# Kernel tuning notes

Hardware: AMD Instinct MI355X
Metric: run time of the kernel (lower is better)

## Reference

```python
import jax, jax.numpy as jnp
import numpy as np

B, F, T, K = 131072, 1024, 100, 32  # batch, num_features, num_trees, features per tree (sqrt(F))


def setup_inputs() -> dict:
    key = jax.random.key(0)
    kx, kw = jax.random.split(key)
    x = jax.random.normal(kx, (B, F), dtype=jnp.float32)
    # per-tree random feature selection without replacement (np.random.choice replace=False)
    rng = np.random.default_rng(0)
    idx = np.argsort(rng.random((T, F)), axis=1)[:, :K].astype(np.int32)
    feature_indices = jnp.asarray(idx)
    feature_thresholds = jnp.zeros((T, K), dtype=jnp.float32)  # lazy-init zeros in original
    feature_weights = jax.random.uniform(kw, (T, K), dtype=jnp.float32)  # torch.rand
    return {
        "x": x,
        "feature_indices": feature_indices,
        "feature_thresholds": feature_thresholds,
        "feature_weights": feature_weights,
    }


def reference(x, feature_indices, feature_thresholds, feature_weights):
    # Per tree t: ws_t = sum_k (x[:, idx[t,k]] - thr[t,k]) * w[t,k]
    # Equivalent fused form: scatter weights into a dense [T, F] matrix and do one GEMM,
    # with per-tree bias sum_k thr*w. scatter-add handles any duplicate indices identically
    # to the gather-then-sum formulation.
    T_, K_ = feature_indices.shape
    tree_ids = jnp.arange(T_, dtype=feature_indices.dtype)[:, None]  # [T,1]
    W_full = jnp.zeros((T_, x.shape[1]), dtype=x.dtype).at[tree_ids, feature_indices].add(feature_weights)
    bias = jnp.sum(feature_thresholds * feature_weights, axis=1)  # [T]
    ws = x @ W_full.T - bias[None, :]  # [B, T]
    p = jax.nn.sigmoid(ws)
    pm = jnp.mean(p, axis=1)  # mean over trees; mean(1-p) = 1 - mean(p)
    return jnp.stack([1.0 - pm, pm], axis=1)  # [B, 2]
```

## Files before the change

### kernel.cpp

```cpp
#include <hip/hip_runtime.h>
#include <math.h>

constexpr int Bn = 131072;
constexpr int Fn = 1024;
constexpr int Tn = 100;
constexpr int Kn = 32;

constexpr int TP = 112;
constexpr int NF = TP / 16;
constexpr int BK = 64;
constexpr int KS = BK / 32;
constexpr int NT = Fn / BK;
constexpr int BM = 128;
constexpr int MW = 32;
constexpr int BLOCK = 256;
constexpr int GRID = Bn / BM;

typedef __attribute__((ext_vector_type(8))) short bf16x8;
typedef __attribute__((ext_vector_type(4))) float f32x4;

using gptr_t = const __attribute__((address_space(1))) void*;
using lptr_t = __attribute__((address_space(3))) void*;

__device__ inline unsigned short f2bf(float f) {
    uint32_t u = __float_as_uint(f);
    return (unsigned short)((u + 0x7FFFu + ((u >> 16) & 1u)) >> 16);
}

__global__ __launch_bounds__(64)
void rf_prep(const int* __restrict__ fidx, const float* __restrict__ fthr,
             const float* __restrict__ fw,
             unsigned short* __restrict__ wt, float* __restrict__ bias)
{
    const int t    = blockIdx.x;
    const int lane = threadIdx.x;

    int4 z = make_int4(0, 0, 0, 0);
    int4* rowp = (int4*)(wt + (size_t)t * Fn);
    rowp[lane * 2 + 0] = z;
    rowp[lane * 2 + 1] = z;
    __syncthreads();

    float bsum = 0.f;
    if (t < Tn && lane < Kn) {
        const int   idx = fidx[t * Kn + lane];
        const float w   = fw[t * Kn + lane];
        const float th  = fthr[t * Kn + lane];
        wt[(size_t)t * Fn + idx] = f2bf(w);
        bsum = th * w;
    }
#pragma unroll
    for (int d = 1; d < 64; d <<= 1) bsum += __shfl_xor(bsum, d, 64);
    if (lane == 0) bias[t] = (t < Tn) ? bsum : 0.f;
}

__global__ __launch_bounds__(BLOCK, 2)
void rf_gemm(const float* __restrict__ x,
             const unsigned short* __restrict__ wt,
             const float* __restrict__ bias,
             float* __restrict__ out)
{
    __shared__ float lds[2][BM * BK];

    const int lane = threadIdx.x & 63;
    const int wid  = threadIdx.x >> 6;
    const int rb   = blockIdx.x * BM;

    const int s_r = lane >> 4;
    const int s_p = lane & 15;
    const int a_L = lane & 15;
    const int a_g = lane >> 4;

    f32x4 acc[2][NF];
#pragma unroll
    for (int m = 0; m < 2; ++m)
#pragma unroll
        for (int f = 0; f < NF; ++f) acc[m][f] = (f32x4){0.f, 0.f, 0.f, 0.f};

    auto stage = [&](int t, int bsel) {
#pragma unroll
        for (int i = 0; i < 8; ++i) {
            const int row = i * 4 + s_r;
            const int c   = s_p ^ (row & 15);
            const float* src = x + (size_t)(rb + wid * MW + row) * Fn + t * BK + c * 4;
            float* dst = &lds[bsel][wid * (MW * BK) + i * 256];
            __builtin_amdgcn_global_load_lds((gptr_t)src, (lptr_t)dst, 16, 0, 0);
        }
    };

    auto loadB = [&](int t, bf16x8 (&bfr)[KS][NF]) {
#pragma unroll
        for (int ks = 0; ks < KS; ++ks)
#pragma unroll
            for (int f = 0; f < NF; ++f) {
                const unsigned short* bp =
                    wt + (size_t)(f * 16 + a_L) * Fn + t * BK + ks * 32 + a_g * 8;
                bfr[ks][f] = *(const bf16x8*)bp;
            }
    };

    auto readA = [&](int bsel, bf16x8 (&af)[KS][2]) {
        const float* buf = &lds[bsel][wid * (MW * BK)];
#pragma unroll
        for (int ks = 0; ks < KS; ++ks)
#pragma unroll
            for (int m = 0; m < 2; ++m) {
                const float* rp = buf + (m * 16 + a_L) * BK;
                const int c0 = ks * 8 + a_g * 2;
                float4 lo = *(const float4*)(rp + ((c0 ^ a_L) * 4));
                float4 hi = *(const float4*)(rp + (((c0 + 1) ^ a_L) * 4));
                bf16x8 v;
                v[0] = (short)f2bf(lo.x); v[1] = (short)f2bf(lo.y);
                v[2] = (short)f2bf(lo.z); v[3] = (short)f2bf(lo.w);
                v[4] = (short)f2bf(hi.x); v[5] = (short)f2bf(hi.y);
                v[6] = (short)f2bf(hi.z); v[7] = (short)f2bf(hi.w);
                af[ks][m] = v;
            }
    };

    auto mfma_all = [&](bf16x8 (&af)[KS][2], bf16x8 (&bfr)[KS][NF]) {
#pragma unroll
        for (int ks = 0; ks < KS; ++ks)
#pragma unroll
            for (int m = 0; m < 2; ++m)
#pragma unroll
                for (int f = 0; f < NF; ++f)
                    acc[m][f] = __builtin_amdgcn_mfma_f32_16x16x32_bf16(
                        af[ks][m], bfr[ks][f], acc[m][f], 0, 0, 0);
    };

    bf16x8 bA[KS][NF], bB[KS][NF];
    bf16x8 af[KS][2];

    stage(0, 0);
    __builtin_amdgcn_sched_barrier(0);
    loadB(0, bA);
    __builtin_amdgcn_sched_barrier(0);
    stage(1, 1);

    for (int t = 0; t < NT; t += 2) {
        loadB(t + 1, bB);
        asm volatile("s_waitcnt vmcnt(36)" ::: "memory");
        readA(0, af);
        asm volatile("s_waitcnt lgkmcnt(0)" ::: "memory");
        if (t + 2 < NT) stage(t + 2, 0);
        mfma_all(af, bA);

        if (t + 2 < NT) {
            loadB(t + 2, bA);
            asm volatile("s_waitcnt vmcnt(36)" ::: "memory");
        } else {
            asm volatile("s_waitcnt vmcnt(14)" ::: "memory");
        }
        readA(1, af);
        asm volatile("s_waitcnt lgkmcnt(0)" ::: "memory");
        if (t + 3 < NT) stage(t + 3, 1);
        mfma_all(af, bB);
    }

    const int col = lane & 15;
    float psum[2][4] = {};
#pragma unroll
    for (int f = 0; f < NF; ++f) {
        const int  n     = f * 16 + col;
        const bool valid = n < Tn;
        const float bv   = bias[n];
#pragma unroll
        for (int m = 0; m < 2; ++m)
#pragma unroll
            for (int r = 0; r < 4; ++r) {
                const float ws = acc[m][f][r] - bv;
                const float p  = 1.f / (1.f + __expf(-ws));
                if (valid) psum[m][r] += p;
            }
    }
#pragma unroll
    for (int m = 0; m < 2; ++m)
#pragma unroll
        for (int r = 0; r < 4; ++r)
#pragma unroll
            for (int d = 1; d < 16; d <<= 1)
                psum[m][r] += __shfl_xor(psum[m][r], d, 64);

    const int g = lane >> 4;
#pragma unroll
    for (int m = 0; m < 2; ++m) {
        if (col < 4) {
            const int r   = col;
            const int row = rb + wid * MW + m * 16 + g * 4 + r;
            const float pm = psum[m][r] * (1.0f / Tn);
            *(float2*)(out + (size_t)row * 2) = make_float2(1.0f - pm, pm);
        }
    }
}

extern "C" void kernel_launch(void* const* d_in, const int* in_sizes, int n_in,
                              void* d_out, int out_size, void* d_ws, size_t ws_size,
                              hipStream_t stream) {
    const float* x    = (const float*)d_in[0];
    const int*   fidx = (const int*)  d_in[1];
    const float* fthr = (const float*)d_in[2];
    const float* fw   = (const float*)d_in[3];
    float*       out  = (float*)d_out;

    unsigned short* wt   = (unsigned short*)d_ws;
    float*          bias = (float*)((char*)d_ws + (size_t)TP * Fn * 2);

    rf_prep<<<TP, 64, 0, stream>>>(fidx, fthr, fw, wt, bias);
    rf_gemm<<<GRID, BLOCK, 0, stream>>>(x, wt, bias, out);
}
```

Baseline: 159.3 us.

## Stage A through registers instead of direct global-to-LDS loads, stagger tile order

Replaces the global_load_lds staging of x tiles with ordinary global loads into registers followed by explicit LDS stores, rebuilding the software pipeline around register-held prefetches with new waitcnt thresholds. Each block also starts its K loop at a different tile offset so concurrent blocks spread their reads over different columns of x and the weight matrix. B fragments are now loaded into a single buffer just before use, and A is converted per k-step. This raises register pressure and removes the explicit syncthreads-free direct LDS path. The hand-tuned vmcnt counts may not match the new load counts.

```diff
diff --git a/kernel.cpp b/kernel.cpp
--- a/kernel.cpp
+++ b/kernel.cpp
@@ -19,9 +19,6 @@
 typedef __attribute__((ext_vector_type(8))) short bf16x8;
 typedef __attribute__((ext_vector_type(4))) float f32x4;
 
-using gptr_t = const __attribute__((address_space(1))) void*;
-using lptr_t = __attribute__((address_space(3))) void*;
-
 __device__ inline unsigned short f2bf(float f) {
     uint32_t u = __float_as_uint(f);
     return (unsigned short)((u + 0x7FFFu + ((u >> 16) & 1u)) >> 16);
@@ -65,97 +62,110 @@
     const int lane = threadIdx.x & 63;
     const int wid  = threadIdx.x >> 6;
     const int rb   = blockIdx.x * BM;
-
-    const int s_r = lane >> 4;
-    const int s_p = lane & 15;
+    const int tofs = blockIdx.x & (NT - 1);
+
+    const int s_sub = lane >> 4;
+    const int s_c   = lane & 15;
     const int a_L = lane & 15;
     const int a_g = lane >> 4;
 
+    int waddr[8];
+#pragma unroll
+    for (int i = 0; i < 8; ++i) {
+        const int row  = i * 4 + s_sub;
+        const int phys = s_c ^ (row & 15);
+        waddr[i] = wid * (MW * BK * 4) + row * (BK * 4) + phys * 16;
+    }
+
     f32x4 acc[2][NF];
 #pragma unroll
     for (int m = 0; m < 2; ++m)
 #pragma unroll
         for (int f = 0; f < NF; ++f) acc[m][f] = (f32x4){0.f, 0.f, 0.f, 0.f};
 
-    auto stage = [&](int t, int bsel) {
-#pragma unroll
-        for (int i = 0; i < 8; ++i) {
-            const int row = i * 4 + s_r;
-            const int c   = s_p ^ (row & 15);
-            const float* src = x + (size_t)(rb + wid * MW + row) * Fn + t * BK + c * 4;
-            float* dst = &lds[bsel][wid * (MW * BK) + i * 256];
-            __builtin_amdgcn_global_load_lds((gptr_t)src, (lptr_t)dst, 16, 0, 0);
-        }
+    auto tileof = [&](int t) { return (t + tofs) & (NT - 1); };
+
+    auto issueA = [&](int t, float4 (&R)[8]) {
+        const float* base = x + (size_t)(rb + wid * MW) * Fn + tileof(t) * BK;
+#pragma unroll
+        for (int i = 0; i < 8; ++i)
+            R[i] = *(const float4*)(base + (size_t)(i * 4 + s_sub) * Fn + s_c * 4);
+    };
+
+    auto writeA = [&](const float4 (&R)[8], int bsel) {
+        char* lp = (char*)&lds[0][0] + bsel * (BM * BK * 4);
+#pragma unroll
+        for (int i = 0; i < 8; ++i)
+            *(float4*)(lp + waddr[i]) = R[i];
     };
 
     auto loadB = [&](int t, bf16x8 (&bfr)[KS][NF]) {
+        const int tp = tileof(t);
 #pragma unroll
         for (int ks = 0; ks < KS; ++ks)
 #pragma unroll
             for (int f = 0; f < NF; ++f) {
                 const unsigned short* bp =
-                    wt + (size_t)(f * 16 + a_L) * Fn + t * BK + ks * 32 + a_g * 8;
+                    wt + (size_t)(f * 16 + a_L) * Fn + tp * BK + ks * 32 + a_g * 8;
                 bfr[ks][f] = *(const bf16x8*)bp;
             }
     };
 
-    auto readA = [&](int bsel, bf16x8 (&af)[KS][2]) {
-        const float* buf = &lds[bsel][wid * (MW * BK)];
-#pragma unroll
-        for (int ks = 0; ks < KS; ++ks)
+    auto compute = [&](int bsel, bf16x8 (&bfr)[KS][NF]) {
+        const char* lp = (const char*)&lds[0][0] + bsel * (BM * BK * 4)
+                       + wid * (MW * BK * 4);
+#pragma unroll
+        for (int ks = 0; ks < KS; ++ks) {
+            bf16x8 af[2];
 #pragma unroll
             for (int m = 0; m < 2; ++m) {
-                const float* rp = buf + (m * 16 + a_L) * BK;
+                const char* rp = lp + (m * 16 + a_L) * (BK * 4);
                 const int c0 = ks * 8 + a_g * 2;
-                float4 lo = *(const float4*)(rp + ((c0 ^ a_L) * 4));
-                float4 hi = *(const float4*)(rp + (((c0 + 1) ^ a_L) * 4));
+                float4 lo = *(const float4*)(rp + ((c0 ^ a_L) * 16));
+                float4 hi = *(const float4*)(rp + (((c0 + 1) ^ a_L) * 16));
                 bf16x8 v;
                 v[0] = (short)f2bf(lo.x); v[1] = (short)f2bf(lo.y);
                 v[2] = (short)f2bf(lo.z); v[3] = (short)f2bf(lo.w);
                 v[4] = (short)f2bf(hi.x); v[5] = (short)f2bf(hi.y);
                 v[6] = (short)f2bf(hi.z); v[7] = (short)f2bf(hi.w);
-                af[ks][m] = v;
+                af[m] = v;
             }
-    };
-
-    auto mfma_all = [&](bf16x8 (&af)[KS][2], bf16x8 (&bfr)[KS][NF]) {
-#pragma unroll
-        for (int ks = 0; ks < KS; ++ks)
 #pragma unroll
             for (int m = 0; m < 2; ++m)
 #pragma unroll
                 for (int f = 0; f < NF; ++f)
                     acc[m][f] = __builtin_amdgcn_mfma_f32_16x16x32_bf16(
-                        af[ks][m], bfr[ks][f], acc[m][f], 0, 0, 0);
-    };
-
-    bf16x8 bA[KS][NF], bB[KS][NF];
-    bf16x8 af[KS][2];
-
-    stage(0, 0);
-    __builtin_amdgcn_sched_barrier(0);
-    loadB(0, bA);
-    __builtin_amdgcn_sched_barrier(0);
-    stage(1, 1);
+                        af[m], bfr[ks][f], acc[m][f], 0, 0, 0);
+        }
+    };
+
+    float4 Ra[8], Rb[8];
+    bf16x8 breg[KS][NF];
+
+    issueA(0, Ra);
+    writeA(Ra, 0);
+    issueA(1, Ra);
 
     for (int t = 0; t < NT; t += 2) {
-        loadB(t + 1, bB);
-        asm volatile("s_waitcnt vmcnt(36)" ::: "memory");
-        readA(0, af);
-        asm volatile("s_waitcnt lgkmcnt(0)" ::: "memory");
-        if (t + 2 < NT) stage(t + 2, 0);
-        mfma_all(af, bA);
-
+        loadB(t, breg);
         if (t + 2 < NT) {
-            loadB(t + 2, bA);
-            asm volatile("s_waitcnt vmcnt(36)" ::: "memory");
+            issueA(t + 2, Rb);
+            asm volatile("s_waitcnt vmcnt(22)" ::: "memory");
         } else {
             asm volatile("s_waitcnt vmcnt(14)" ::: "memory");
         }
-        readA(1, af);
-        asm volatile("s_waitcnt lgkmcnt(0)" ::: "memory");
-        if (t + 3 < NT) stage(t + 3, 1);
-        mfma_all(af, bB);
+        writeA(Ra, (t + 1) & 1);
+        compute(t & 1, breg);
+
+        loadB(t + 1, breg);
+        if (t + 3 < NT) {
+            issueA(t + 3, Ra);
+            asm volatile("s_waitcnt vmcnt(22)" ::: "memory");
+        } else if (t + 2 < NT) {
+            asm volatile("s_waitcnt vmcnt(14)" ::: "memory");
+        }
+        if (t + 2 < NT) writeA(Rb, (t + 2) & 1);
+        compute((t + 1) & 1, breg);
     }
 
     const int col = lane & 15;
```

New measurement: 297.3 us. +86.6%, slower.
